# Kernel tuning notes

Measured on AMD Instinct MI355X. Metric: run time of the kernel, lower is better.

The kernel has to match this reference:

```python
import jax, jax.numpy as jnp
import numpy as np
from jax import lax

B, S, D_IN, D_STATE, D_OUT, N_HEADS = 4, 2048, 2048, 2048, 2048, 16
H = D_STATE // N_HEADS  # 128


def setup_inputs() -> dict:
    key = jax.random.key(0)
    k1, k2, k3, k4, k5 = jax.random.split(key, 5)
    x = jax.random.normal(k1, (B, S, D_IN), dtype=jnp.float32)
    Wi = jax.random.normal(k2, (D_IN, D_STATE), dtype=jnp.float32) * (D_IN ** -0.5)
    b = jax.random.normal(k3, (D_STATE,), dtype=jnp.float32) * 0.01
    # state_weight is init'd with normal_ in torch; scale down for numerical sanity
    state_w = jax.random.normal(k4, (N_HEADS, H, H), dtype=jnp.float32) * (H ** -0.5)
    Wo = jax.random.normal(k5, (D_STATE, D_OUT), dtype=jnp.float32) * (D_STATE ** -0.5)
    input_state = jnp.zeros((B, D_STATE), dtype=jnp.float32)
    return {"x": x, "input_state": input_state, "Wi": Wi, "b": b,
            "state_w": state_w, "Wo": Wo}


def _rnn_forward(x, input_state, Wi, b, state_w, Wo):
    # input projection: [B,S,D_IN] -> [B,S,N,H]
    xp = (jnp.einsum('bsd,de->bse', x, Wi) + b).reshape(B, S, N_HEADS, H)
    h0 = input_state.reshape(B, N_HEADS, H)

    def step(h, xt):  # h: [B,N,H], xt: [B,N,H]
        h = jnp.tanh(jnp.einsum('bnh,nhk->bnk', h, state_w) + xt)
        return h, h

    _, hs = lax.scan(step, h0, jnp.moveaxis(xp, 1, 0))  # hs: [S,B,N,H]
    hs = jnp.moveaxis(hs, 0, 1)                         # [B,S,N,H]
    output_state = hs[:, -1].reshape(B, D_STATE)        # [B, state_size]
    out = jnp.einsum('bsd,de->bse', hs.reshape(B, S, D_STATE), Wo)
    return out, output_state


def reference(x, input_state, Wi, b, state_w, Wo):
    return _rnn_forward(x, input_state, Wi, b, state_w, Wo)
```

## Files before the change

kernel.cpp:

```cpp
#include <hip/hip_runtime.h>
#include <hip/hip_bf16.h>

#define B_ 4
#define S_ 2048
#define DIN 2048
#define DST 2048
#define DOUT 2048
#define NH 16
#define HH 128
#define M_ (B_ * S_)
#define OUT_OFF ((size_t)M_ * DOUT)

typedef __attribute__((ext_vector_type(8))) __bf16 bf16x8;
typedef __attribute__((ext_vector_type(4))) float f32x4;
typedef __attribute__((ext_vector_type(2))) _Float16 f16x2;

__device__ __forceinline__ unsigned short f2bf(float f) {
    unsigned int u = __float_as_uint(f);
    unsigned int r = u + 0x7FFFu + ((u >> 16) & 1u);
    return (unsigned short)(r >> 16);
}

__device__ __forceinline__ float fdot2(f16x2 a, f16x2 b, float c) {
#if __has_builtin(__builtin_amdgcn_fdot2)
    return __builtin_amdgcn_fdot2(a, b, c, false);
#else
    return fmaf((float)a.x, (float)b.x, fmaf((float)a.y, (float)b.y, c));
#endif
}

#define DPP_PULL(v, ctrl) __builtin_bit_cast(float, \
    __builtin_amdgcn_mov_dpp(__builtin_bit_cast(int, (v)), (ctrl), 0xf, 0xf, true))

__device__ __forceinline__ void gload_lds16(const void* g, void* l) {
    __builtin_amdgcn_global_load_lds(
        (const __attribute__((address_space(1))) void*)g,
        (__attribute__((address_space(3))) void*)l, 16, 0, 0);
}

__global__ __launch_bounds__(256) void k_cast_bf16(
    const float* __restrict__ in, unsigned short* __restrict__ out, int n8) {
    int i = blockIdx.x * 256 + threadIdx.x;
    if (i >= n8) return;
    const float4* p = ((const float4*)in) + (size_t)i * 2;
    float4 a = p[0], b = p[1];
    ushort4 r0, r1;
    r0.x = f2bf(a.x); r0.y = f2bf(a.y); r0.z = f2bf(a.z); r0.w = f2bf(a.w);
    r1.x = f2bf(b.x); r1.y = f2bf(b.y); r1.z = f2bf(b.z); r1.w = f2bf(b.w);
    ushort4* o = ((ushort4*)out) + (size_t)i * 2;
    o[0] = r0; o[1] = r1;
}

__global__ __launch_bounds__(256) void k_transpose_bf16(
    const float* __restrict__ in, unsigned short* __restrict__ out, int K, int N) {
    __shared__ float tile[64][65];
    int k0 = blockIdx.y * 64, n0 = blockIdx.x * 64;
    int tr  = threadIdx.x >> 4;
    int tc4 = (threadIdx.x & 15) * 4;
#pragma unroll
    for (int p = 0; p < 4; ++p) {
        int r = tr + p * 16;
        float4 v = *(const float4*)&in[(size_t)(k0 + r) * N + n0 + tc4];
        tile[r][tc4 + 0] = v.x; tile[r][tc4 + 1] = v.y;
        tile[r][tc4 + 2] = v.z; tile[r][tc4 + 3] = v.w;
    }
    __syncthreads();
#pragma unroll
    for (int p = 0; p < 4; ++p) {
        int n = tr + p * 16;
        ushort4 o;
        o.x = f2bf(tile[tc4 + 0][n]); o.y = f2bf(tile[tc4 + 1][n]);
        o.z = f2bf(tile[tc4 + 2][n]); o.w = f2bf(tile[tc4 + 3][n]);
        *(ushort4*)&out[(size_t)(n0 + n) * K + k0 + tc4] = o;
    }
}

__global__ __launch_bounds__(256, 2) void k_gemm_bt(
    const unsigned short* __restrict__ A,
    const unsigned short* __restrict__ Bt,
    float* __restrict__ C,
    const float* __restrict__ bias,
    int M, int N, int K, int hasBias) {
    __shared__ unsigned short As[128 * 64];
    __shared__ unsigned short Bs[128 * 64];
    const int tid  = threadIdx.x;
    const int lane = tid & 63;
    const int wid  = tid >> 6;
    const int wr = wid >> 1, wc = wid & 1;
    const int row0 = blockIdx.y * 128, col0 = blockIdx.x * 128;

    f32x4 acc[4][4];
#pragma unroll
    for (int m = 0; m < 4; ++m)
#pragma unroll
        for (int n = 0; n < 4; ++n) acc[m][n] = (f32x4)(0.f);

    const char* Abase = (const char*)(A + (size_t)row0 * K);
    const char* Bbase = (const char*)(Bt + (size_t)col0 * K);

    int srow[4], skb[4];
#pragma unroll
    for (int i = 0; i < 4; ++i) {
        unsigned o = (unsigned)(i * 256 + tid) * 16u;
        unsigned l = o ^ (((o >> 7) & 7u) << 4);
        srow[i] = (int)(l >> 7);
        skb[i]  = (int)(l & 127u);
    }

    for (int kt = 0; kt < K; kt += 64) {
#pragma unroll
        for (int i = 0; i < 4; ++i) {
            unsigned o = (unsigned)(i * 256 + tid) * 16u;
            gload_lds16(Abase + (size_t)srow[i] * (K * 2) + (size_t)kt * 2 + skb[i],
                        (char*)As + o);
            gload_lds16(Bbase + (size_t)srow[i] * (K * 2) + (size_t)kt * 2 + skb[i],
                        (char*)Bs + o);
        }
        asm volatile("s_waitcnt vmcnt(0)" ::: "memory");
        __syncthreads();
#pragma unroll
        for (int ks = 0; ks < 2; ++ks) {
            bf16x8 af[4], bfr[4];
#pragma unroll
            for (int m = 0; m < 4; ++m) {
                int row = wr * 64 + m * 16 + (lane & 15);
                unsigned o = (unsigned)(row * 128 + ks * 64 + ((lane >> 4) * 16));
                o ^= ((unsigned)(row & 7) << 4);
                af[m] = *(const bf16x8*)((const char*)As + o);
            }
#pragma unroll
            for (int n = 0; n < 4; ++n) {
                int col = wc * 64 + n * 16 + (lane & 15);
                unsigned o = (unsigned)(col * 128 + ks * 64 + ((lane >> 4) * 16));
                o ^= ((unsigned)(col & 7) << 4);
                bfr[n] = *(const bf16x8*)((const char*)Bs + o);
            }
#pragma unroll
            for (int m = 0; m < 4; ++m)
#pragma unroll
                for (int n = 0; n < 4; ++n)
                    acc[m][n] = __builtin_amdgcn_mfma_f32_16x16x32_bf16(
                        af[m], bfr[n], acc[m][n], 0, 0, 0);
        }
        __syncthreads();
    }

#pragma unroll
    for (int n = 0; n < 4; ++n) {
        int gcol = col0 + wc * 64 + n * 16 + (lane & 15);
        float bv = hasBias ? bias[gcol] : 0.f;
#pragma unroll
        for (int m = 0; m < 4; ++m) {
            int growb = row0 + wr * 64 + m * 16 + ((lane >> 4) * 4);
            float* cp = C + (size_t)growb * N + gcol;
#pragma unroll
            for (int r = 0; r < 4; ++r) cp[(size_t)r * N] = acc[m][n][r] + bv;
        }
    }
}

__global__ __attribute__((amdgpu_flat_work_group_size(256, 256),
                          amdgpu_waves_per_eu(1, 1))) void k_scan(
    const float* __restrict__ xp,
    const float* __restrict__ h0,
    const float* __restrict__ sw,
    unsigned short* __restrict__ hsb,
    float* __restrict__ out_state) {
    __shared__ __align__(16) unsigned hb[2][64];
    const int tid  = threadIdx.x;
    const int lane = tid & 63;
    const int wv   = tid >> 6;
    const int G    = wv * 16 + (lane >> 2);
    const int q    = lane & 3;
    const int col0 = G * 2;
    const int bb = blockIdx.x >> 4;
    const int nn = blockIdx.x & 15;

    const float* wbp = sw + (size_t)nn * HH * HH + (size_t)(q * 32) * HH + col0;
#define MKW(j) f16x2 wA##j, wB##j; { const float* pw = wbp + (size_t)(2 * (j)) * HH; \
        wA##j = f16x2{(_Float16)pw[0], (_Float16)pw[HH]};                            \
        wB##j = f16x2{(_Float16)pw[1], (_Float16)pw[HH + 1]}; }
    MKW(0)  MKW(1)  MKW(2)  MKW(3)  MKW(4)  MKW(5)  MKW(6)  MKW(7)
    MKW(8)  MKW(9)  MKW(10) MKW(11) MKW(12) MKW(13) MKW(14) MKW(15)
#undef MKW

    if (tid < 64) {
        float2 h2 = *(const float2*)(h0 + bb * DST + nn * HH + 2 * tid);
        unsigned lo = __builtin_bit_cast(unsigned short, (_Float16)h2.x);
        unsigned hi = __builtin_bit_cast(unsigned short, (_Float16)h2.y);
        hb[0][tid] = lo | (hi << 16);
    }

    const float2* xrow2 = (const float2*)(xp + (size_t)bb * S_ * DST + nn * HH) + G;
    unsigned* hcol32 = (unsigned*)(hsb + (size_t)bb * S_ * DST + nn * HH) + G;
    float* osp = out_state + bb * DST + nn * HH + col0;

    float2 xq0 = xrow2[0];
    float2 xq1 = xrow2[(size_t)1 * (DST / 2)];
    float2 xq2 = xrow2[(size_t)2 * (DST / 2)];
    float2 xq3 = xrow2[(size_t)3 * (DST / 2)];

    asm volatile("s_waitcnt lgkmcnt(0)\ns_barrier" ::: "memory");

    int p = 0;
    for (int t = 0; t < S_; ++t) {
        int tp = (t + 4 < S_) ? t + 4 : S_ - 1;
        float2 xq4 = xrow2[(size_t)tp * (DST / 2)];

        const uint4* hp = (const uint4*)&hb[p][q * 16];
        uint4 Ra = hp[0], Rb = hp[1], Rc = hp[2], Rd = hp[3];

        float a0e = 0.f, a0o = 0.f, a1e = 0.f, a1o = 0.f;
#define D2(u, j, s) { f16x2 hj = __builtin_bit_cast(f16x2, (unsigned)(u)); \
        a0##s = fdot2(hj, wA##j, a0##s); a1##s = fdot2(hj, wB##j, a1##s); }
        D2(Ra.x, 0,  e) D2(Ra.y, 1,  o) D2(Ra.z, 2,  e) D2(Ra.w, 3,  o)
        D2(Rb.x, 4,  e) D2(Rb.y, 5,  o) D2(Rb.z, 6,  e) D2(Rb.w, 7,  o)
        D2(Rc.x, 8,  e) D2(Rc.y, 9,  o) D2(Rc.z, 10, e) D2(Rc.w, 11, o)
        D2(Rd.x, 12, e) D2(Rd.y, 13, o) D2(Rd.z, 14, e) D2(Rd.w, 15, o)
#undef D2
        float r0 = a0e + a0o;
        float r1 = a1e + a1o;
        r0 += DPP_PULL(r0, 0xB1); r0 += DPP_PULL(r0, 0x4E);
        r1 += DPP_PULL(r1, 0xB1); r1 += DPP_PULL(r1, 0x4E);

        float s0 = r0 + xq0.x;
        float s1 = r1 + xq0.y;
        float ssel = (lane & 1) ? s1 : s0;
        float e = __builtin_amdgcn_exp2f(ssel * 2.885390081777927f);
        float th = fmaf(-2.f, __builtin_amdgcn_rcpf(e + 1.f), 1.f);
        float uo = DPP_PULL(th, 0xB1);

        if (q == 0) {
            unsigned lo16 = __builtin_bit_cast(unsigned short, (_Float16)th);
            unsigned hi16 = __builtin_bit_cast(unsigned short, (_Float16)uo);
            hb[p ^ 1][G] = lo16 | (hi16 << 16);
            hcol32[(size_t)t * (DST / 2)] = (unsigned)f2bf(th) | ((unsigned)f2bf(uo) << 16);
            if (t == S_ - 1) { osp[0] = th; osp[1] = uo; }
        }
        asm volatile("s_waitcnt lgkmcnt(0)\ns_barrier" ::: "memory");
        p ^= 1;
        xq0 = xq1; xq1 = xq2; xq2 = xq3; xq3 = xq4;
    }
}

extern "C" void kernel_launch(void* const* d_in, const int* in_sizes, int n_in,
                              void* d_out, int out_size, void* d_ws, size_t ws_size,
                              hipStream_t stream) {
    const float* x    = (const float*)d_in[0];
    const float* h0   = (const float*)d_in[1];
    const float* Wi   = (const float*)d_in[2];
    const float* bias = (const float*)d_in[3];
    const float* sw   = (const float*)d_in[4];
    const float* Wo   = (const float*)d_in[5];
    float* out = (float*)d_out;

    char* ws = (char*)d_ws;
    unsigned short* xb  = (unsigned short*)ws;
    unsigned short* wit = (unsigned short*)(ws + 33554432);
    unsigned short* wot = (unsigned short*)(ws + 41943040);
    float*          xp  = (float*)(ws + 50331648);

    k_cast_bf16<<<8192, 256, 0, stream>>>(x, xb, (M_ * DIN) / 8);
    dim3 tg(32, 32);
    k_transpose_bf16<<<tg, 256, 0, stream>>>(Wi, wit, DIN, DST);
    k_transpose_bf16<<<tg, 256, 0, stream>>>(Wo, wot, DST, DOUT);
    dim3 g1(DST / 128, M_ / 128);
    k_gemm_bt<<<g1, 256, 0, stream>>>(xb, wit, xp, bias, M_, DST, DIN, 1);
    k_scan<<<B_ * NH, 256, 0, stream>>>(xp, h0, sw, xb, out + OUT_OFF);
    dim3 g2(DOUT / 128, M_ / 128);
    k_gemm_bt<<<g2, 256, 0, stream>>>(xb, wot, out, nullptr, M_, DOUT, DST, 0);
}
```

Baseline: 863.6 us.

## Fuse input GEMM, scan and output GEMM into persistent kernel with flag pipelining

Replaces the separate cast, input GEMM, scan and output GEMM launches with one persistent kernel. 64 blocks run the recurrence, 96 compute the input projection chunk by chunk, and 96 compute the output projection. Flags in global memory let the scan start as soon as its time chunk is projected and let the output GEMM consume hidden states chunk by chunk. The projection is stored as fp16 instead of fp32, and x is converted to bf16 inside the GEMM, so the separate cast pass goes away. The cost is a deadlock risk if all 256 blocks are not co-resident, and only 96 blocks are left for each GEMM.

```diff
diff --git a/kernel.cpp b/kernel.cpp
--- a/kernel.cpp
+++ b/kernel.cpp
@@ -11,6 +11,12 @@
 #define M_ (B_ * S_)
 #define OUT_OFF ((size_t)M_ * DOUT)
 
+#define WS_HS    0u
+#define WS_WIT   33554432u
+#define WS_WOT   41943040u
+#define WS_XP    50331648u
+#define WS_FLAGS 83886080u
+
 typedef __attribute__((ext_vector_type(8))) __bf16 bf16x8;
 typedef __attribute__((ext_vector_type(4))) float f32x4;
 typedef __attribute__((ext_vector_type(2))) _Float16 f16x2;
@@ -38,17 +44,12 @@
         (__attribute__((address_space(3))) void*)l, 16, 0, 0);
 }
 
-__global__ __launch_bounds__(256) void k_cast_bf16(
-    const float* __restrict__ in, unsigned short* __restrict__ out, int n8) {
-    int i = blockIdx.x * 256 + threadIdx.x;
-    if (i >= n8) return;
-    const float4* p = ((const float4*)in) + (size_t)i * 2;
-    float4 a = p[0], b = p[1];
-    ushort4 r0, r1;
-    r0.x = f2bf(a.x); r0.y = f2bf(a.y); r0.z = f2bf(a.z); r0.w = f2bf(a.w);
-    r1.x = f2bf(b.x); r1.y = f2bf(b.y); r1.z = f2bf(b.z); r1.w = f2bf(b.w);
-    ushort4* o = ((ushort4*)out) + (size_t)i * 2;
-    o[0] = r0; o[1] = r1;
+__device__ __forceinline__ void wait_flag(const unsigned* p, unsigned v) {
+    if (threadIdx.x == 0) {
+        while (__hip_atomic_load(p, __ATOMIC_ACQUIRE, __HIP_MEMORY_SCOPE_AGENT) < v)
+            __builtin_amdgcn_s_sleep(8);
+    }
+    __syncthreads();
 }
 
 __global__ __launch_bounds__(256) void k_transpose_bf16(
@@ -75,29 +76,118 @@
     }
 }
 
-__global__ __launch_bounds__(256, 2) void k_gemm_bt(
-    const unsigned short* __restrict__ A,
-    const unsigned short* __restrict__ Bt,
-    float* __restrict__ C,
+__global__ __attribute__((amdgpu_flat_work_group_size(256, 256),
+                          amdgpu_waves_per_eu(1, 1))) void k_mega(
+    const float* __restrict__ x,
+    const float* __restrict__ h0,
+    const float* __restrict__ sw,
     const float* __restrict__ bias,
-    int M, int N, int K, int hasBias) {
+    const unsigned short* __restrict__ wit,
+    const unsigned short* __restrict__ wot,
+    unsigned short* __restrict__ xpf,
+    unsigned short* __restrict__ hs,
+    float* __restrict__ out,
+    float* __restrict__ out_state,
+    unsigned* __restrict__ flags1,
+    unsigned* __restrict__ flags2) {
     __shared__ unsigned short As[128 * 64];
     __shared__ unsigned short Bs[128 * 64];
-    const int tid  = threadIdx.x;
+    __shared__ __align__(16) unsigned hb[2][64];
+    const int blk = blockIdx.x;
+    const int tid = threadIdx.x;
     const int lane = tid & 63;
     const int wid  = tid >> 6;
-    const int wr = wid >> 1, wc = wid & 1;
-    const int row0 = blockIdx.y * 128, col0 = blockIdx.x * 128;
-
-    f32x4 acc[4][4];
-#pragma unroll
-    for (int m = 0; m < 4; ++m)
-#pragma unroll
-        for (int n = 0; n < 4; ++n) acc[m][n] = (f32x4)(0.f);
-
-    const char* Abase = (const char*)(A + (size_t)row0 * K);
-    const char* Bbase = (const char*)(Bt + (size_t)col0 * K);
-
+
+    if (blk < 64) {
+        const int G  = wid * 16 + (lane >> 2);
+        const int q  = lane & 3;
+        const int c0 = G * 2;
+        const int bb = blk >> 4;
+        const int nn = blk & 15;
+
+        const float* wbp = sw + (size_t)nn * HH * HH + (size_t)(q * 32) * HH + c0;
+#define MKW(j) f16x2 wA##j, wB##j; { const float* pw = wbp + (size_t)(2 * (j)) * HH; \
+        wA##j = f16x2{(_Float16)pw[0], (_Float16)pw[HH]};                            \
+        wB##j = f16x2{(_Float16)pw[1], (_Float16)pw[HH + 1]}; }
+        MKW(0)  MKW(1)  MKW(2)  MKW(3)  MKW(4)  MKW(5)  MKW(6)  MKW(7)
+        MKW(8)  MKW(9)  MKW(10) MKW(11) MKW(12) MKW(13) MKW(14) MKW(15)
+#undef MKW
+
+        if (tid < 64) {
+            float2 h2 = *(const float2*)(h0 + bb * DST + nn * HH + 2 * tid);
+            unsigned lo = __builtin_bit_cast(unsigned short, (_Float16)h2.x);
+            unsigned hi = __builtin_bit_cast(unsigned short, (_Float16)h2.y);
+            hb[0][tid] = lo | (hi << 16);
+        }
+
+        const unsigned* xH = (const unsigned*)(xpf + (size_t)bb * S_ * DST + nn * HH) + G;
+        unsigned* hrow32 = (unsigned*)(hs + (size_t)bb * S_ * DST + nn * HH) + G;
+        float* osp = out_state + bb * DST + nn * HH + c0;
+
+        wait_flag(&flags1[0 * 64 + bb * 16 + nn], 1);
+        wait_flag(&flags1[1 * 64 + bb * 16 + nn], 1);
+
+        unsigned xh0 = xH[0], xh1 = xH[1024], xh2 = xH[2048], xh3 = xH[3072];
+
+        asm volatile("s_waitcnt lgkmcnt(0)\ns_barrier" ::: "memory");
+
+        int p = 0;
+        for (int c = 0; c < 16; ++c) {
+            if (c >= 1) {
+                int cn = (c + 1 > 15) ? 15 : c + 1;
+                wait_flag(&flags1[cn * 64 + bb * 16 + nn], 1);
+            }
+            for (int tt = 0; tt < 128; ++tt) {
+                int t = c * 128 + tt;
+                int tpf = (t + 4 < S_) ? t + 4 : S_ - 1;
+                unsigned xh4 = xH[(size_t)tpf * 1024];
+
+                const uint4* hp = (const uint4*)&hb[p][q * 16];
+                uint4 Ra = hp[0], Rb = hp[1], Rc = hp[2], Rd = hp[3];
+
+                float a0e = 0.f, a0o = 0.f, a1e = 0.f, a1o = 0.f;
+#define D2(u, j, s) { f16x2 hj = __builtin_bit_cast(f16x2, (unsigned)(u)); \
+        a0##s = fdot2(hj, wA##j, a0##s); a1##s = fdot2(hj, wB##j, a1##s); }
+                D2(Ra.x, 0,  e) D2(Ra.y, 1,  o) D2(Ra.z, 2,  e) D2(Ra.w, 3,  o)
+                D2(Rb.x, 4,  e) D2(Rb.y, 5,  o) D2(Rb.z, 6,  e) D2(Rb.w, 7,  o)
+                D2(Rc.x, 8,  e) D2(Rc.y, 9,  o) D2(Rc.z, 10, e) D2(Rc.w, 11, o)
+                D2(Rd.x, 12, e) D2(Rd.y, 13, o) D2(Rd.z, 14, e) D2(Rd.w, 15, o)
+#undef D2
+                float r0 = a0e + a0o;
+                float r1 = a1e + a1o;
+                r0 += DPP_PULL(r0, 0xB1); r0 += DPP_PULL(r0, 0x4E);
+                r1 += DPP_PULL(r1, 0xB1); r1 += DPP_PULL(r1, 0x4E);
+
+                f16x2 xv = __builtin_bit_cast(f16x2, xh0);
+                float s0 = r0 + (float)xv.x;
+                float s1 = r1 + (float)xv.y;
+                float ssel = (lane & 1) ? s1 : s0;
+                float e = __builtin_amdgcn_exp2f(ssel * 2.885390081777927f);
+                float th = fmaf(-2.f, __builtin_amdgcn_rcpf(e + 1.f), 1.f);
+                float uo = DPP_PULL(th, 0xB1);
+
+                if (q == 0) {
+                    unsigned lo16 = __builtin_bit_cast(unsigned short, (_Float16)th);
+                    unsigned hi16 = __builtin_bit_cast(unsigned short, (_Float16)uo);
+                    hb[p ^ 1][G] = lo16 | (hi16 << 16);
+                    hrow32[(size_t)t * (DST / 2)] =
+                        (unsigned)f2bf(th) | ((unsigned)f2bf(uo) << 16);
+                    if (t == S_ - 1) { osp[0] = th; osp[1] = uo; }
+                }
+                asm volatile("s_waitcnt lgkmcnt(0)\ns_barrier" ::: "memory");
+                p ^= 1;
+                xh0 = xh1; xh1 = xh2; xh2 = xh3; xh3 = xh4;
+            }
+            asm volatile("s_waitcnt vmcnt(0)" ::: "memory");
+            __syncthreads();
+            if (tid == 0)
+                __hip_atomic_fetch_add(&flags2[bb * 16 + c], 1u,
+                                       __ATOMIC_RELEASE, __HIP_MEMORY_SCOPE_AGENT);
+        }
+        return;
+    }
+
+    const int wr = (wid >> 1), wc = (wid & 1);
     int srow[4], skb[4];
 #pragma unroll
     for (int i = 0; i < 4; ++i) {
@@ -107,139 +197,152 @@
         skb[i]  = (int)(l & 127u);
     }
 
-    for (int kt = 0; kt < K; kt += 64) {
-#pragma unroll
-        for (int i = 0; i < 4; ++i) {
-            unsigned o = (unsigned)(i * 256 + tid) * 16u;
-            gload_lds16(Abase + (size_t)srow[i] * (K * 2) + (size_t)kt * 2 + skb[i],
-                        (char*)As + o);
-            gload_lds16(Bbase + (size_t)srow[i] * (K * 2) + (size_t)kt * 2 + skb[i],
-                        (char*)Bs + o);
+    if (blk < 160) {
+        const int w = blk - 64;
+        for (int T = w; T < 1024; T += 96) {
+            int c = T >> 6, b = (T >> 4) & 3, n = T & 15;
+            int row0 = b * 2048 + c * 128, col0 = n * 128;
+            const float* Ab = x + (size_t)row0 * DIN;
+            const char* Bb = (const char*)(wit + (size_t)col0 * DIN);
+
+            f32x4 acc[4][4];
+#pragma unroll
+            for (int m = 0; m < 4; ++m)
+#pragma unroll
+                for (int nn2 = 0; nn2 < 4; ++nn2) acc[m][nn2] = (f32x4)(0.f);
+
+            for (int kt = 0; kt < DIN; kt += 64) {
+#pragma unroll
+                for (int i = 0; i < 8; ++i) {
+                    int idx = i * 256 + tid;
+                    int row = idx >> 4;
+                    int cc  = (idx & 15) * 4;
+                    float4 v = *(const float4*)&Ab[(size_t)row * DIN + kt + cc];
+                    ushort4 u;
+                    u.x = f2bf(v.x); u.y = f2bf(v.y); u.z = f2bf(v.z); u.w = f2bf(v.w);
+                    unsigned byte = (unsigned)(row * 128 + cc * 2);
+                    byte ^= ((unsigned)(row & 7)) << 4;
+                    *(ushort4*)((char*)As + byte) = u;
+                }
+#pragma unroll
+                for (int i = 0; i < 4; ++i) {
+                    unsigned o = (unsigned)(i * 256 + tid) * 16u;
+                    gload_lds16(Bb + (size_t)srow[i] * (DIN * 2) + (size_t)kt * 2 + skb[i],
+                                (char*)Bs + o);
+                }
+                asm volatile("s_waitcnt vmcnt(0)" ::: "memory");
+                __syncthreads();
+#pragma unroll
+                for (int ks = 0; ks < 2; ++ks) {
+                    bf16x8 af[4], bfr[4];
+#pragma unroll
+                    for (int m = 0; m < 4; ++m) {
+                        int row = wr * 64 + m * 16 + (lane & 15);
+                        unsigned o = (unsigned)(row * 128 + ks * 64 + ((lane >> 4) * 16));
+                        o ^= ((unsigned)(row & 7) << 4);
+                        af[m] = *(const bf16x8*)((const char*)As + o);
+                    }
+#pragma unroll
+                    for (int nn2 = 0; nn2 < 4; ++nn2) {
+                        int col = wc * 64 + nn2 * 16 + (lane & 15);
+                        unsigned o = (unsigned)(col * 128 + ks * 64 + ((lane >> 4) * 16));
+                        o ^= ((unsigned)(col & 7) << 4);
+                        bfr[nn2] = *(const bf16x8*)((const char*)Bs + o);
+                    }
+#pragma unroll
+                    for (int m = 0; m < 4; ++m)
+#pragma unroll
+                        for (int nn2 = 0; nn2 < 4; ++nn2)
+                            acc[m][nn2] = __builtin_amdgcn_mfma_f32_16x16x32_bf16(
+                                af[m], bfr[nn2], acc[m][nn2], 0, 0, 0);
+                }
+                __syncthreads();
+            }
+#pragma unroll
+            for (int nn2 = 0; nn2 < 4; ++nn2) {
+                int gcol = col0 + wc * 64 + nn2 * 16 + (lane & 15);
+                float bv = bias[gcol];
+#pragma unroll
+                for (int m = 0; m < 4; ++m) {
+                    int growb = row0 + wr * 64 + m * 16 + ((lane >> 4) * 4);
+#pragma unroll
+                    for (int r = 0; r < 4; ++r) {
+                        float v = acc[m][nn2][r] + bv;
+                        xpf[(size_t)(growb + r) * DST + gcol] =
+                            __builtin_bit_cast(unsigned short, (_Float16)v);
+                    }
+                }
+            }
+            asm volatile("s_waitcnt vmcnt(0)" ::: "memory");
+            __syncthreads();
+            if (tid == 0)
+                __hip_atomic_store(&flags1[T], 1u,
+                                   __ATOMIC_RELEASE, __HIP_MEMORY_SCOPE_AGENT);
         }
-        asm volatile("s_waitcnt vmcnt(0)" ::: "memory");
-        __syncthreads();
-#pragma unroll
-        for (int ks = 0; ks < 2; ++ks) {
-            bf16x8 af[4], bfr[4];
-#pragma unroll
-            for (int m = 0; m < 4; ++m) {
-                int row = wr * 64 + m * 16 + (lane & 15);
-                unsigned o = (unsigned)(row * 128 + ks * 64 + ((lane >> 4) * 16));
-                o ^= ((unsigned)(row & 7) << 4);
-                af[m] = *(const bf16x8*)((const char*)As + o);
-            }
-#pragma unroll
-            for (int n = 0; n < 4; ++n) {
-                int col = wc * 64 + n * 16 + (lane & 15);
-                unsigned o = (unsigned)(col * 128 + ks * 64 + ((lane >> 4) * 16));
-                o ^= ((unsigned)(col & 7) << 4);
-                bfr[n] = *(const bf16x8*)((const char*)Bs + o);
-            }
+    } else {
+        const int w = blk - 160;
+        for (int T = w; T < 1024; T += 96) {
+            int c = T >> 6, b = (T >> 4) & 3, ct = T & 15;
+            wait_flag(&flags2[b * 16 + c], 16);
+            int row0 = b * 2048 + c * 128, col0 = ct * 128;
+            const char* Abase = (const char*)(hs + (size_t)row0 * DST);
+            const char* Bbase = (const char*)(wot + (size_t)col0 * DST);
+
+            f32x4 acc[4][4];
 #pragma unroll
             for (int m = 0; m < 4; ++m)
 #pragma unroll
-                for (int n = 0; n < 4; ++n)
-                    acc[m][n] = __builtin_amdgcn_mfma_f32_16x16x32_bf16(
-                        af[m], bfr[n], acc[m][n], 0, 0, 0);
+                for (int nn2 = 0; nn2 < 4; ++nn2) acc[m][nn2] = (f32x4)(0.f);
+
+            for (int kt = 0; kt < DST; kt += 64) {
+#pragma unroll
+                for (int i = 0; i < 4; ++i) {
+                    unsigned o = (unsigned)(i * 256 + tid) * 16u;
+                    gload_lds16(Abase + (size_t)srow[i] * (DST * 2) + (size_t)kt * 2 + skb[i],
+                                (char*)As + o);
+                    gload_lds16(Bbase + (size_t)srow[i] * (DST * 2) + (size_t)kt * 2 + skb[i],
+                                (char*)Bs + o);
+                }
+                asm volatile("s_waitcnt vmcnt(0)" ::: "memory");
+                __syncthreads();
+#pragma unroll
+                for (int ks = 0; ks < 2; ++ks) {
+                    bf16x8 af[4], bfr[4];
+#pragma unroll
+                    for (int m = 0; m < 4; ++m) {
+                        int row = wr * 64 + m * 16 + (lane & 15);
+                        unsigned o = (unsigned)(row * 128 + ks * 64 + ((lane >> 4) * 16));
+                        o ^= ((unsigned)(row & 7) << 4);
+                        af[m] = *(const bf16x8*)((const char*)As + o);
+                    }
+#pragma unroll
+                    for (int nn2 = 0; nn2 < 4; ++nn2) {
+                        int col = wc * 64 + nn2 * 16 + (lane & 15);
+                        unsigned o = (unsigned)(col * 128 + ks * 64 + ((lane >> 4) * 16));
+                        o ^= ((unsigned)(col & 7) << 4);
+                        bfr[nn2] = *(const bf16x8*)((const char*)Bs + o);
+                    }
+#pragma unroll
+                    for (int m = 0; m < 4; ++m)
+#pragma unroll
+                        for (int nn2 = 0; nn2 < 4; ++nn2)
+                            acc[m][nn2] = __builtin_amdgcn_mfma_f32_16x16x32_bf16(
+                                af[m], bfr[nn2], acc[m][nn2], 0, 0, 0);
+                }
+                __syncthreads();
+            }
+#pragma unroll
+            for (int nn2 = 0; nn2 < 4; ++nn2) {
+                int gcol = col0 + wc * 64 + nn2 * 16 + (lane & 15);
+#pragma unroll
+                for (int m = 0; m < 4; ++m) {
+                    int growb = row0 + wr * 64 + m * 16 + ((lane >> 4) * 4);
+                    float* cp = out + (size_t)growb * DOUT + gcol;
+#pragma unroll
+                    for (int r = 0; r < 4; ++r) cp[(size_t)r * DOUT] = acc[m][nn2][r];
+                }
+            }
         }
-        __syncthreads();
-    }
-
-#pragma unroll
-    for (int n = 0; n < 4; ++n) {
-        int gcol = col0 + wc * 64 + n * 16 + (lane & 15);
-        float bv = hasBias ? bias[gcol] : 0.f;
-#pragma unroll
-        for (int m = 0; m < 4; ++m) {
-            int growb = row0 + wr * 64 + m * 16 + ((lane >> 4) * 4);
-            float* cp = C + (size_t)growb * N + gcol;
-#pragma unroll
-            for (int r = 0; r < 4; ++r) cp[(size_t)r * N] = acc[m][n][r] + bv;
-        }
-    }
-}
-
-__global__ __attribute__((amdgpu_flat_work_group_size(256, 256),
-                          amdgpu_waves_per_eu(1, 1))) void k_scan(
-    const float* __restrict__ xp,
-    const float* __restrict__ h0,
-    const float* __restrict__ sw,
-    unsigned short* __restrict__ hsb,
-    float* __restrict__ out_state) {
-    __shared__ __align__(16) unsigned hb[2][64];
-    const int tid  = threadIdx.x;
-    const int lane = tid & 63;
-    const int wv   = tid >> 6;
-    const int G    = wv * 16 + (lane >> 2);
-    const int q    = lane & 3;
-    const int col0 = G * 2;
-    const int bb = blockIdx.x >> 4;
-    const int nn = blockIdx.x & 15;
-
-    const float* wbp = sw + (size_t)nn * HH * HH + (size_t)(q * 32) * HH + col0;
-#define MKW(j) f16x2 wA##j, wB##j; { const float* pw = wbp + (size_t)(2 * (j)) * HH; \
-        wA##j = f16x2{(_Float16)pw[0], (_Float16)pw[HH]};                            \
-        wB##j = f16x2{(_Float16)pw[1], (_Float16)pw[HH + 1]}; }
-    MKW(0)  MKW(1)  MKW(2)  MKW(3)  MKW(4)  MKW(5)  MKW(6)  MKW(7)
-    MKW(8)  MKW(9)  MKW(10) MKW(11) MKW(12) MKW(13) MKW(14) MKW(15)
-#undef MKW
-
-    if (tid < 64) {
-        float2 h2 = *(const float2*)(h0 + bb * DST + nn * HH + 2 * tid);
-        unsigned lo = __builtin_bit_cast(unsigned short, (_Float16)h2.x);
-        unsigned hi = __builtin_bit_cast(unsigned short, (_Float16)h2.y);
-        hb[0][tid] = lo | (hi << 16);
-    }
-
-    const float2* xrow2 = (const float2*)(xp + (size_t)bb * S_ * DST + nn * HH) + G;
-    unsigned* hcol32 = (unsigned*)(hsb + (size_t)bb * S_ * DST + nn * HH) + G;
-    float* osp = out_state + bb * DST + nn * HH + col0;
-
-    float2 xq0 = xrow2[0];
-    float2 xq1 = xrow2[(size_t)1 * (DST / 2)];
-    float2 xq2 = xrow2[(size_t)2 * (DST / 2)];
-    float2 xq3 = xrow2[(size_t)3 * (DST / 2)];
-
-    asm volatile("s_waitcnt lgkmcnt(0)\ns_barrier" ::: "memory");
-
-    int p = 0;
-    for (int t = 0; t < S_; ++t) {
-        int tp = (t + 4 < S_) ? t + 4 : S_ - 1;
-        float2 xq4 = xrow2[(size_t)tp * (DST / 2)];
-
-        const uint4* hp = (const uint4*)&hb[p][q * 16];
-        uint4 Ra = hp[0], Rb = hp[1], Rc = hp[2], Rd = hp[3];
-
-        float a0e = 0.f, a0o = 0.f, a1e = 0.f, a1o = 0.f;
-#define D2(u, j, s) { f16x2 hj = __builtin_bit_cast(f16x2, (unsigned)(u)); \
-        a0##s = fdot2(hj, wA##j, a0##s); a1##s = fdot2(hj, wB##j, a1##s); }
-        D2(Ra.x, 0,  e) D2(Ra.y, 1,  o) D2(Ra.z, 2,  e) D2(Ra.w, 3,  o)
-        D2(Rb.x, 4,  e) D2(Rb.y, 5,  o) D2(Rb.z, 6,  e) D2(Rb.w, 7,  o)
-        D2(Rc.x, 8,  e) D2(Rc.y, 9,  o) D2(Rc.z, 10, e) D2(Rc.w, 11, o)
-        D2(Rd.x, 12, e) D2(Rd.y, 13, o) D2(Rd.z, 14, e) D2(Rd.w, 15, o)
-#undef D2
-        float r0 = a0e + a0o;
-        float r1 = a1e + a1o;
-        r0 += DPP_PULL(r0, 0xB1); r0 += DPP_PULL(r0, 0x4E);
-        r1 += DPP_PULL(r1, 0xB1); r1 += DPP_PULL(r1, 0x4E);
-
-        float s0 = r0 + xq0.x;
-        float s1 = r1 + xq0.y;
-        float ssel = (lane & 1) ? s1 : s0;
-        float e = __builtin_amdgcn_exp2f(ssel * 2.885390081777927f);
-        float th = fmaf(-2.f, __builtin_amdgcn_rcpf(e + 1.f), 1.f);
-        float uo = DPP_PULL(th, 0xB1);
-
-        if (q == 0) {
-            unsigned lo16 = __builtin_bit_cast(unsigned short, (_Float16)th);
-            unsigned hi16 = __builtin_bit_cast(unsigned short, (_Float16)uo);
-            hb[p ^ 1][G] = lo16 | (hi16 << 16);
-            hcol32[(size_t)t * (DST / 2)] = (unsigned)f2bf(th) | ((unsigned)f2bf(uo) << 16);
-            if (t == S_ - 1) { osp[0] = th; osp[1] = uo; }
-        }
-        asm volatile("s_waitcnt lgkmcnt(0)\ns_barrier" ::: "memory");
-        p ^= 1;
-        xq0 = xq1; xq1 = xq2; xq2 = xq3; xq3 = xq4;
     }
 }
 
@@ -255,18 +358,18 @@
     float* out = (float*)d_out;
 
     char* ws = (char*)d_ws;
-    unsigned short* xb  = (unsigned short*)ws;
-    unsigned short* wit = (unsigned short*)(ws + 33554432);
-    unsigned short* wot = (unsigned short*)(ws + 41943040);
-    float*          xp  = (float*)(ws + 50331648);
-
-    k_cast_bf16<<<8192, 256, 0, stream>>>(x, xb, (M_ * DIN) / 8);
+    unsigned short* hsb = (unsigned short*)(ws + WS_HS);
+    unsigned short* wit = (unsigned short*)(ws + WS_WIT);
+    unsigned short* wot = (unsigned short*)(ws + WS_WOT);
+    unsigned short* xpf = (unsigned short*)(ws + WS_XP);
+    unsigned* flags1 = (unsigned*)(ws + WS_FLAGS);
+    unsigned* flags2 = flags1 + 1024;
+
     dim3 tg(32, 32);
     k_transpose_bf16<<<tg, 256, 0, stream>>>(Wi, wit, DIN, DST);
     k_transpose_bf16<<<tg, 256, 0, stream>>>(Wo, wot, DST, DOUT);
-    dim3 g1(DST / 128, M_ / 128);
-    k_gemm_bt<<<g1, 256, 0, stream>>>(xb, wit, xp, bias, M_, DST, DIN, 1);
-    k_scan<<<B_ * NH, 256, 0, stream>>>(xp, h0, sw, xb, out + OUT_OFF);
-    dim3 g2(DOUT / 128, M_ / 128);
-    k_gemm_bt<<<g2, 256, 0, stream>>>(xb, wot, out, nullptr, M_, DOUT, DST, 0);
-}
+    hipMemsetAsync(ws + WS_FLAGS, 0, 8192, stream);
+    k_mega<<<256, 256, 0, stream>>>(x, h0, sw, bias, wit, wot,
+                                    xpf, hsb, out, out + OUT_OFF,
+                                    flags1, flags2);
+}
```

New measurement: 1.305 ms. 1.51x slower.
